# Optimization experiments

Hardware: AMD Instinct MI355X
Metric: run time of the kernel (lower is better)

## Reference

```python
import jax, jax.numpy as jnp
import numpy as np

B, T, H = 1, 2048, 2048
HEADS, DH = 16, 128  # head_dim = H // HEADS
K = 50               # block size
NEG = -1e9


def setup_inputs() -> dict:
    key = jax.random.key(0)
    ks = jax.random.split(key, 6)
    x = jax.random.normal(ks[0], (B, T, H), jnp.float32)
    mask = jnp.ones((B, T), jnp.float32)
    bias = jax.random.normal(ks[1], (B, HEADS, T, T), jnp.float32) * 0.02
    s = 1.0 / np.sqrt(H)
    Wq = jax.random.normal(ks[2], (H, HEADS, DH), jnp.float32) * s
    Wk = jax.random.normal(ks[3], (H, HEADS, DH), jnp.float32) * s
    Wv = jax.random.normal(ks[4], (H, HEADS, DH), jnp.float32) * s
    Wo = jax.random.normal(ks[5], (HEADS, DH, H), jnp.float32) * (1.0 / np.sqrt(H))
    return {"x_BxTxH": x, "mask_BxT": mask, "attention_bias_BxHxTxT": bias,
            "Wq": Wq, "Wk": Wk, "Wv": Wv, "Wo": Wo}


def _local_self_attention(x, mask, bias, Wq, Wk, Wv, Wo):
    b, t, h = x.shape
    extra = K - t % K          # module always pads (pads a full block if t % K == 0)
    p = t + extra
    n = p // K
    # pad + block the inputs: [b, n, K, h]
    xb = jnp.pad(x, ((0, 0), (0, extra), (0, 0))).reshape(b, n, K, h)
    # pad mask with -1e9 (as in the module), block, build pairwise mask via multiply
    mb = jnp.pad(mask, ((0, 0), (0, extra)), constant_values=NEG).reshape(b, n, K)
    pair = mb[..., :, None] * mb[..., None, :]              # [b, n, K, K]
    mask_bias = jnp.where(pair > 0, 0.0, NEG)[:, :, None]   # [b, n, 1, K, K] (broadcast heads)
    # pad attention bias and extract block-diagonal: [b, n, heads, K, K]
    bp = jnp.pad(bias, ((0, 0), (0, 0), (0, extra), (0, extra)))
    nb = bp.reshape(b, HEADS, n, K, n, K)
    idx = jnp.arange(n)
    blk_bias = nb[:, :, idx, :, idx, :]          # [n, b, heads, K, K]
    blk_bias = jnp.transpose(blk_bias, (1, 0, 2, 3, 4))  # [b, n, heads, K, K]
    # per-block multi-head attention (no qkv bias, query scaled by head_dim**-0.5)
    q = jnp.einsum('bnkh,hef->bnkef', xb, Wq) * (DH ** -0.5)
    k = jnp.einsum('bnkh,hef->bnkef', xb, Wk)
    v = jnp.einsum('bnkh,hef->bnkef', xb, Wv)
    logits = jnp.einsum('bnqef,bnkef->bneqk', q, k) + blk_bias + mask_bias
    attn = jax.nn.softmax(logits, axis=-1)
    out = jnp.einsum('bneqk,bnkef->bnqef', attn, v)
    out = jnp.einsum('bnqef,efh->bnqh', out, Wo).reshape(b, p, h)
    return out[:, :t, :]


def reference(x_BxTxH, mask_BxT, attention_bias_BxHxTxT, Wq, Wk, Wv, Wo):
    return _local_self_attention(x_BxTxH, mask_BxT, attention_bias_BxHxTxT, Wq, Wk, Wv, Wo)
```

## Files before the change

kernel.cpp:

```cpp
#include <hip/hip_runtime.h>
#include <hip/hip_bf16.h>

typedef _Float16 f16x8 __attribute__((ext_vector_type(8)));
typedef float f32x4 __attribute__((ext_vector_type(4)));

#define T_DIM 2048
#define H_DIM 2048
#define N_HEADS 16
#define DH 128
#define KBLK 50
#define NBLK 41
#define NEGV (-1.0e9f)
#define QSCALE 0.08838834764831845f

__device__ __forceinline__ void gl_lds16(const void* g, void* l) {
    __builtin_amdgcn_global_load_lds(
        (const __attribute__((address_space(1))) void*)g,
        (__attribute__((address_space(3))) void*)l, 16, 0, 0);
}

__global__ __launch_bounds__(256) void prep_kernel(const float* __restrict__ x,
                                                   const float* __restrict__ Wq,
                                                   const float* __restrict__ Wk,
                                                   const float* __restrict__ Wv,
                                                   const float* __restrict__ Wo,
                                                   _Float16* __restrict__ xb,
                                                   _Float16* __restrict__ WT,
                                                   _Float16* __restrict__ WoT) {
    __shared__ float tile[32][33];
    int z = blockIdx.z;
    int tx = threadIdx.x, ty = threadIdx.y;
    if (z == 4) {
        if (blockIdx.y >= 32) return;
        int flat = blockIdx.y * 64 + blockIdx.x;
        int i = (flat * 256 + ty * 32 + tx) * 8;
        float4 a = *(const float4*)&x[i];
        float4 b = *(const float4*)&x[i + 4];
        f16x8 o = {(_Float16)a.x, (_Float16)a.y, (_Float16)a.z, (_Float16)a.w,
                   (_Float16)b.x, (_Float16)b.y, (_Float16)b.z, (_Float16)b.w};
        *(f16x8*)&xb[i] = o;
        return;
    }
    const float* src = (z == 0) ? Wq : (z == 1) ? Wk : (z == 2) ? Wv : Wo;
    _Float16* dst = (z == 3) ? WoT : (WT + (size_t)z * T_DIM * H_DIM);
    int bx = blockIdx.x * 32, by = blockIdx.y * 32;
#pragma unroll
    for (int i = 0; i < 4; i++)
        tile[ty + i * 8][tx] = src[(size_t)(by + ty + i * 8) * H_DIM + bx + tx];
    __syncthreads();
#pragma unroll
    for (int i = 0; i < 4; i++)
        dst[(size_t)(bx + ty + i * 8) * H_DIM + by + tx] = (_Float16)tile[tx][ty + i * 8];
}

__global__ __launch_bounds__(512, 2) void qkv192_kernel(const _Float16* __restrict__ A,
                                                        const _Float16* __restrict__ BT,
                                                        _Float16* __restrict__ qkv) {
    const int K = 2048, NT = 32;
    __shared__ _Float16 smem[57344];
    _Float16* sA0 = smem;
    _Float16* sA1 = smem + 16384;
    _Float16* sB0 = smem + 32768;
    _Float16* sB1 = smem + 45056;

    int tid = threadIdx.x;
    int lane = tid & 63, wave = tid >> 6;
    int wm = wave >> 2, wn = wave & 3;
    int cb = lane & 15, hi = lane >> 4;

    int bid = blockIdx.x;
    int swz = (bid & 7) * 32 + (bid >> 3);
    int by = swz >> 5, bx = swz & 31;
    int bm = by * 256, bn = bx * 192;

    f32x4 acc[8][3];
#pragma unroll
    for (int m = 0; m < 8; m++)
#pragma unroll
        for (int n = 0; n < 3; n++) acc[m][n] = (f32x4){0.f, 0.f, 0.f, 0.f};

    int rp = tid >> 3, cc = tid & 7;
    int scol = ((cc ^ (rp & 7)) << 3);

    auto stageA = [&](int t, int u) {
        int buf = t & 1;
        gl_lds16(A + (size_t)(bm + u * 64 + rp) * K + (t << 6) + scol,
                 (buf ? sA1 : sA0) + u * 4096 + tid * 8);
    };
    auto stageB = [&](int t, int u) {
        int buf = t & 1;
        gl_lds16(BT + (size_t)(bn + u * 64 + rp) * K + (t << 6) + scol,
                 (buf ? sB1 : sB0) + u * 4096 + tid * 8);
    };

    f16x8 a_lo[4][2], a_hi[4][2], b01[2][2], b2[2];

    stageA(0, 0); stageA(0, 1); stageA(0, 2); stageA(0, 3);
    stageB(0, 0); stageB(0, 1); stageB(0, 2);
    stageA(1, 0); stageA(1, 1); stageA(1, 2); stageA(1, 3);
    asm volatile("s_waitcnt vmcnt(4)" ::: "memory");
    __builtin_amdgcn_s_barrier();

    for (int t = 0; t < NT; t++) {
        int buf = t & 1;
        const char* bA = (const char*)(buf ? sA1 : sA0);
        const char* bB = (const char*)(buf ? sB1 : sB0);
#pragma unroll
        for (int mf = 0; mf < 4; mf++) {
            int ra = wm * 128 + mf * 16 + cb;
#pragma unroll
            for (int ks = 0; ks < 2; ks++)
                a_lo[mf][ks] = *(const f16x8*)(bA + (ra << 7) +
                                               ((ks * 64 + hi * 16) ^ ((ra & 7) << 4)));
        }
#pragma unroll
        for (int nf = 0; nf < 2; nf++) {
            int rb = wn * 48 + nf * 16 + cb;
#pragma unroll
            for (int ks = 0; ks < 2; ks++)
                b01[nf][ks] = *(const f16x8*)(bB + (rb << 7) +
                                              ((ks * 64 + hi * 16) ^ ((rb & 7) << 4)));
        }
        if (t + 1 < NT) { stageB(t + 1, 0); stageB(t + 1, 1); }
        __builtin_amdgcn_s_barrier();
        asm volatile("s_waitcnt lgkmcnt(0)" ::: "memory");
        __builtin_amdgcn_s_setprio(1);
#pragma unroll
        for (int mf = 0; mf < 4; mf++)
#pragma unroll
            for (int nf = 0; nf < 2; nf++)
#pragma unroll
                for (int ks = 0; ks < 2; ks++)
                    acc[mf][nf] = __builtin_amdgcn_mfma_f32_16x16x32_f16(a_lo[mf][ks], b01[nf][ks], acc[mf][nf], 0, 0, 0);
        __builtin_amdgcn_s_setprio(0);
        __builtin_amdgcn_s_barrier();

#pragma unroll
        for (int mf = 0; mf < 4; mf++) {
            int ra = wm * 128 + 64 + mf * 16 + cb;
#pragma unroll
            for (int ks = 0; ks < 2; ks++)
                a_hi[mf][ks] = *(const f16x8*)(bA + (ra << 7) +
                                               ((ks * 64 + hi * 16) ^ ((ra & 7) << 4)));
        }
        {
            int rb = wn * 48 + 32 + cb;
#pragma unroll
            for (int ks = 0; ks < 2; ks++)
                b2[ks] = *(const f16x8*)(bB + (rb << 7) +
                                         ((ks * 64 + hi * 16) ^ ((rb & 7) << 4)));
        }
        if (t + 1 < NT) stageB(t + 1, 2);
        __builtin_amdgcn_s_barrier();
        asm volatile("s_waitcnt lgkmcnt(0)" ::: "memory");
        __builtin_amdgcn_s_setprio(1);
#pragma unroll
        for (int mf = 0; mf < 4; mf++)
#pragma unroll
            for (int ks = 0; ks < 2; ks++)
                acc[4 + mf][2] = __builtin_amdgcn_mfma_f32_16x16x32_f16(a_hi[mf][ks], b2[ks], acc[4 + mf][2], 0, 0, 0);
        __builtin_amdgcn_s_setprio(0);
        __builtin_amdgcn_s_barrier();

        if (t + 2 < NT) { stageA(t + 2, 0); stageA(t + 2, 1); }
        __builtin_amdgcn_s_barrier();
        __builtin_amdgcn_s_setprio(1);
#pragma unroll
        for (int mf = 0; mf < 4; mf++)
#pragma unroll
            for (int ks = 0; ks < 2; ks++)
                acc[mf][2] = __builtin_amdgcn_mfma_f32_16x16x32_f16(a_lo[mf][ks], b2[ks], acc[mf][2], 0, 0, 0);
        __builtin_amdgcn_s_setprio(0);
        __builtin_amdgcn_s_barrier();

        if (t + 2 < NT) { stageA(t + 2, 2); stageA(t + 2, 3); }
        if (t < NT - 2)
            asm volatile("s_waitcnt vmcnt(4)" ::: "memory");
        else if (t == NT - 2)
            asm volatile("s_waitcnt vmcnt(0)" ::: "memory");
        __builtin_amdgcn_s_barrier();
        __builtin_amdgcn_s_setprio(1);
#pragma unroll
        for (int mf = 0; mf < 4; mf++)
#pragma unroll
            for (int nf = 0; nf < 2; nf++)
#pragma unroll
                for (int ks = 0; ks < 2; ks++)
                    acc[4 + mf][nf] = __builtin_amdgcn_mfma_f32_16x16x32_f16(a_hi[mf][ks], b01[nf][ks], acc[4 + mf][nf], 0, 0, 0);
        __builtin_amdgcn_s_setprio(0);
        __builtin_amdgcn_s_barrier();
    }

#pragma unroll
    for (int p = 0; p < 2; p++) {
        if (p) __builtin_amdgcn_s_barrier();
        if (wm == p) {
#pragma unroll
            for (int mf = 0; mf < 8; mf++)
#pragma unroll
                for (int nf = 0; nf < 3; nf++) {
                    int col = wn * 48 + nf * 16 + cb;
                    float sc = ((bn + col) >> 11) == 0 ? QSCALE : 1.0f;
#pragma unroll
                    for (int r = 0; r < 4; r++) {
                        int row = mf * 16 + hi * 4 + r;
                        smem[row * 200 + col] = (_Float16)(acc[mf][nf][r] * sc);
                    }
                }
        }
        __builtin_amdgcn_s_barrier();
#pragma unroll
        for (int it = 0; it < 6; it++) {
            int c = it * 512 + tid;
            int row = c / 24, col8 = c - row * 24;
            int gm = bm + p * 128 + row;
            int gn = bn + col8 * 8;
            int tensor = gn >> 11;
            int ef = gn & 2047;
            int e = ef >> 7, f0 = ef & 127;
            uint4 v = *(const uint4*)&smem[row * 200 + col8 * 8];
            *(uint4*)(qkv + (size_t)tensor * (T_DIM * H_DIM) + (size_t)e * (T_DIM * DH) +
                      (size_t)gm * DH + f0) = v;
        }
    }
}

__global__ __launch_bounds__(512, 1) void oproj_kernel(const _Float16* __restrict__ A,
                                                       const _Float16* __restrict__ BT,
                                                       float* __restrict__ out) {
    const int K = 2048, NT = 32;
    __shared__ _Float16 smem[49152];

    int tid = threadIdx.x;
    int lane = tid & 63, wave = tid >> 6;
    int wm = wave >> 2, wn = wave & 3;
    int cb = lane & 15, hi = lane >> 4;

    int bid = blockIdx.x;
    int by = bid >> 4, bx = bid & 15;
    int bm = by * 128, bn = bx * 128;

    f32x4 acc[4][2];
#pragma unroll
    for (int m = 0; m < 4; m++)
#pragma unroll
        for (int n = 0; n < 2; n++) acc[m][n] = (f32x4){0.f, 0.f, 0.f, 0.f};

    int rp = tid >> 3, cc = tid & 7;
    int scol = ((cc ^ (rp & 7)) << 3);

    auto bufp = [&](int t) { return smem + (t % 3) * 16384; };
    auto stageA = [&](int t, int u) {
        gl_lds16(A + (size_t)(bm + u * 64 + rp) * K + (t << 6) + scol,
                 bufp(t) + u * 4096 + tid * 8);
    };
    auto stageB = [&](int t, int u) {
        gl_lds16(BT + (size_t)(bn + u * 64 + rp) * K + (t << 6) + scol,
                 bufp(t) + 8192 + u * 4096 + tid * 8);
    };

    f16x8 a[4][2], b0[2], b1[2];

    stageA(0, 0); stageA(0, 1); stageB(0, 0); stageB(0, 1);
    stageA(1, 0); stageA(1, 1); stageB(1, 0); stageB(1, 1);
    asm volatile("s_waitcnt vmcnt(4)" ::: "memory");
    __builtin_amdgcn_s_barrier();

    for (int t = 0; t < NT; t++) {
        const char* bA = (const char*)bufp(t);
        const char* bB = bA + 16384;
#pragma unroll
        for (int mf = 0; mf < 4; mf++) {
            int ra = wm * 64 + mf * 16 + cb;
#pragma unroll
            for (int ks = 0; ks < 2; ks++)
                a[mf][ks] = *(const f16x8*)(bA + (ra << 7) +
                                            ((ks * 64 + hi * 16) ^ ((ra & 7) << 4)));
        }
        {
            int rb = wn * 32 + cb;
#pragma unroll
            for (int ks = 0; ks < 2; ks++)
                b0[ks] = *(const f16x8*)(bB + (rb << 7) +
                                         ((ks * 64 + hi * 16) ^ ((rb & 7) << 4)));
        }
        if (t + 2 < NT) { stageA(t + 2, 0); stageA(t + 2, 1); }
        __builtin_amdgcn_s_barrier();
        asm volatile("s_waitcnt lgkmcnt(0)" ::: "memory");
        __builtin_amdgcn_s_setprio(1);
#pragma unroll
        for (int mf = 0; mf < 4; mf++)
#pragma unroll
            for (int ks = 0; ks < 2; ks++)
                acc[mf][0] = __builtin_amdgcn_mfma_f32_16x16x32_f16(a[mf][ks], b0[ks], acc[mf][0], 0, 0, 0);
        __builtin_amdgcn_s_setprio(0);
        __builtin_amdgcn_s_barrier();

        {
            int rb = wn * 32 + 16 + cb;
#pragma unroll
            for (int ks = 0; ks < 2; ks++)
                b1[ks] = *(const f16x8*)(bB + (rb << 7) +
                                         ((ks * 64 + hi * 16) ^ ((rb & 7) << 4)));
        }
        if (t + 2 < NT) { stageB(t + 2, 0); stageB(t + 2, 1); }
        if (t < NT - 2)
            asm volatile("s_waitcnt vmcnt(4)" ::: "memory");
        else if (t == NT - 2)
            asm volatile("s_waitcnt vmcnt(0)" ::: "memory");
        __builtin_amdgcn_s_barrier();
        asm volatile("s_waitcnt lgkmcnt(0)" ::: "memory");
        __builtin_amdgcn_s_setprio(1);
#pragma unroll
        for (int mf = 0; mf < 4; mf++)
#pragma unroll
            for (int ks = 0; ks < 2; ks++)
                acc[mf][1] = __builtin_amdgcn_mfma_f32_16x16x32_f16(a[mf][ks], b1[ks], acc[mf][1], 0, 0, 0);
        __builtin_amdgcn_s_setprio(0);
        __builtin_amdgcn_s_barrier();
    }

#pragma unroll
    for (int mf = 0; mf < 4; mf++)
#pragma unroll
        for (int nf = 0; nf < 2; nf++) {
            int gn = bn + wn * 32 + nf * 16 + cb;
#pragma unroll
            for (int r = 0; r < 4; r++) {
                int gm = bm + wm * 64 + mf * 16 + hi * 4 + r;
                out[(size_t)gm * H_DIM + gn] = acc[mf][nf][r];
            }
        }
}

__global__ __launch_bounds__(256) void attn_kernel(const _Float16* __restrict__ qkvb,
                                                   const float* __restrict__ bias,
                                                   const float* __restrict__ mask,
                                                   _Float16* __restrict__ aout) {
    int bid = blockIdx.x;
    int n = bid >> 4, e = bid & 15;
    int t0 = n * KBLK;
    int valid = (T_DIM - t0 < KBLK) ? (T_DIM - t0) : KBLK;

    __shared__ _Float16 Qs[64 * 136];
    __shared__ _Float16 Ks[64 * 136];
    __shared__ _Float16 VTs[128 * 72];
    __shared__ _Float16 Ps[64 * 72];
    __shared__ float maskv[64];

    int tid = threadIdx.x;
    int lane = tid & 63, wave = tid >> 6;
    const _Float16* qp = qkvb + (size_t)e * (T_DIM * DH);
    const _Float16* kp = qkvb + (size_t)(T_DIM * H_DIM) + (size_t)e * (T_DIM * DH);
    const _Float16* vp = qkvb + (size_t)2 * (T_DIM * H_DIM) + (size_t)e * (T_DIM * DH);

#pragma unroll
    for (int i = 0; i < 4; i++) {
        int c = tid + i * 256;
        int r = c >> 4, c8 = c & 15;
        uint4 z = {0u, 0u, 0u, 0u};
        uint4 vq = z, vk = z;
        if (r < valid) {
            vq = *(const uint4*)&qp[(size_t)(t0 + r) * DH + c8 * 8];
            vk = *(const uint4*)&kp[(size_t)(t0 + r) * DH + c8 * 8];
        }
        *(uint4*)&Qs[r * 136 + c8 * 8] = vq;
        *(uint4*)&Ks[r * 136 + c8 * 8] = vk;
    }
#pragma unroll
    for (int i = 0; i < 4; i++) {
        int c = tid + i * 256;
        int r = c & 63;
        int f0 = (c >> 6) * 8;
        uint4 v = {0u, 0u, 0u, 0u};
        if (r < valid) v = *(const uint4*)&vp[(size_t)(t0 + r) * DH + f0];
        _Float16 tmp[8];
        *(uint4*)tmp = v;
#pragma unroll
        for (int j = 0; j < 8; j++) VTs[(f0 + j) * 72 + r] = tmp[j];
    }
    if (tid < 64) maskv[tid] = (tid < valid) ? mask[t0 + tid] : NEGV;
    __syncthreads();

    int qr0 = wave * 16;
    int cb = lane & 15, hi = lane >> 4;

    f16x8 aq[4];
#pragma unroll
    for (int ks = 0; ks < 4; ks++)
        aq[ks] = *(const f16x8*)&Qs[(qr0 + cb) * 136 + ks * 32 + hi * 8];
    f32x4 s[4];
#pragma unroll
    for (int kt = 0; kt < 4; kt++) s[kt] = (f32x4){0.f, 0.f, 0.f, 0.f};
#pragma unroll
    for (int kt = 0; kt < 4; kt++)
#pragma unroll
        for (int ks = 0; ks < 4; ks++) {
            f16x8 bk = *(const f16x8*)&Ks[(kt * 16 + cb) * 136 + ks * 32 + hi * 8];
            s[kt] = __builtin_amdgcn_mfma_f32_16x16x32_f16(aq[ks], bk, s[kt], 0, 0, 0);
        }

#pragma unroll
    for (int r = 0; r < 4; r++) {
        int rl = qr0 + hi * 4 + r;
        int qi = t0 + rl;
        float mq = maskv[rl];
        float lg[4];
        float mx = -3.4e38f;
#pragma unroll
        for (int kt = 0; kt < 4; kt++) {
            int cl = kt * 16 + cb, ki = t0 + cl;
            float bg = (qi < T_DIM && ki < T_DIM)
                           ? bias[((size_t)e * T_DIM + qi) * T_DIM + ki] : 0.f;
            float pr = mq * maskv[cl];
            float v = s[kt][r] + bg + (pr > 0.f ? 0.f : NEGV);
            lg[kt] = v;
            mx = fmaxf(mx, v);
        }
#pragma unroll
        for (int off = 8; off; off >>= 1) mx = fmaxf(mx, __shfl_xor(mx, off));
        float sum = 0.f;
#pragma unroll
        for (int kt = 0; kt < 4; kt++) {
            float pe = __expf(lg[kt] - mx);
            lg[kt] = pe;
            sum += pe;
        }
#pragma unroll
        for (int off = 8; off; off >>= 1) sum += __shfl_xor(sum, off);
        float inv = 1.f / sum;
#pragma unroll
        for (int kt = 0; kt < 4; kt++)
            Ps[rl * 72 + kt * 16 + cb] = (_Float16)(lg[kt] * inv);
    }
    __syncthreads();

    f16x8 pa[2];
#pragma unroll
    for (int ks = 0; ks < 2; ks++)
        pa[ks] = *(const f16x8*)&Ps[(qr0 + cb) * 72 + ks * 32 + hi * 8];
#pragma unroll
    for (int ft = 0; ft < 8; ft++) {
        f32x4 o = (f32x4){0.f, 0.f, 0.f, 0.f};
#pragma unroll
        for (int ks = 0; ks < 2; ks++) {
            f16x8 bv = *(const f16x8*)&VTs[(ft * 16 + cb) * 72 + ks * 32 + hi * 8];
            o = __builtin_amdgcn_mfma_f32_16x16x32_f16(pa[ks], bv, o, 0, 0, 0);
        }
#pragma unroll
        for (int r = 0; r < 4; r++) {
            int rl = qr0 + hi * 4 + r;
            if (rl < valid)
                aout[(size_t)(t0 + rl) * H_DIM + e * DH + ft * 16 + cb] = (_Float16)o[r];
        }
    }
}

extern "C" void kernel_launch(void* const* d_in, const int* in_sizes, int n_in,
                              void* d_out, int out_size, void* d_ws, size_t ws_size,
                              hipStream_t stream) {
    const float* x    = (const float*)d_in[0];
    const float* mask = (const float*)d_in[1];
    const float* bias = (const float*)d_in[2];
    const float* Wq   = (const float*)d_in[3];
    const float* Wk   = (const float*)d_in[4];
    const float* Wv   = (const float*)d_in[5];
    const float* Wo   = (const float*)d_in[6];
    float* out = (float*)d_out;

    _Float16* xb   = (_Float16*)d_ws;
    _Float16* WT   = xb + (size_t)T_DIM * H_DIM;
    _Float16* WoT  = WT + (size_t)3 * T_DIM * H_DIM;
    _Float16* qkvb = WoT + (size_t)T_DIM * H_DIM;
    _Float16* aout = qkvb + (size_t)3 * T_DIM * H_DIM;

    prep_kernel<<<dim3(64, 64, 5), dim3(32, 8), 0, stream>>>(x, Wq, Wk, Wv, Wo, xb, WT, WoT);

    qkv192_kernel<<<256, 512, 0, stream>>>(xb, WT, qkvb);

    attn_kernel<<<NBLK * N_HEADS, 256, 0, stream>>>(qkvb, bias, mask, aout);

    oproj_kernel<<<256, 512, 0, stream>>>(aout, WoT, out);
}
```

Baseline: 119.4 us.

## Shrink QKV and output-projection GEMM tiles to 256-thread blocks with more CTAs

The QKV GEMM moves from 256x192 tiles with 512 threads to 128x192 tiles with 256 threads (2x2 waves, each 64x96). The output projection moves from 128x128 tiles to 128x64 tiles. Both now launch 512 blocks and are tuned for two blocks per CU. The goal is more CTAs, better spread across the GPU's CUs, and less LDS per block, at the cost of lower arithmetic intensity per tile and more global traffic. The QKV block-index swizzle is dropped, and the epilogue is simplified to a single pass through shared memory.

```diff
diff --git a/kernel.cpp b/kernel.cpp
--- a/kernel.cpp
+++ b/kernel.cpp
@@ -53,50 +53,47 @@
         dst[(size_t)(bx + ty + i * 8) * H_DIM + by + tx] = (_Float16)tile[tx][ty + i * 8];
 }
 
-__global__ __launch_bounds__(512, 2) void qkv192_kernel(const _Float16* __restrict__ A,
-                                                        const _Float16* __restrict__ BT,
-                                                        _Float16* __restrict__ qkv) {
+__global__ __launch_bounds__(256, 2) void qkv_kernel(const _Float16* __restrict__ A,
+                                                     const _Float16* __restrict__ BT,
+                                                     _Float16* __restrict__ qkv) {
     const int K = 2048, NT = 32;
-    __shared__ _Float16 smem[57344];
+    __shared__ _Float16 smem[40960];
     _Float16* sA0 = smem;
-    _Float16* sA1 = smem + 16384;
-    _Float16* sB0 = smem + 32768;
-    _Float16* sB1 = smem + 45056;
+    _Float16* sA1 = smem + 8192;
+    _Float16* sB0 = smem + 16384;
+    _Float16* sB1 = smem + 28672;
 
     int tid = threadIdx.x;
     int lane = tid & 63, wave = tid >> 6;
-    int wm = wave >> 2, wn = wave & 3;
+    int wm = wave >> 1, wn = wave & 1;
     int cb = lane & 15, hi = lane >> 4;
 
     int bid = blockIdx.x;
-    int swz = (bid & 7) * 32 + (bid >> 3);
-    int by = swz >> 5, bx = swz & 31;
-    int bm = by * 256, bn = bx * 192;
-
-    f32x4 acc[8][3];
-#pragma unroll
-    for (int m = 0; m < 8; m++)
-#pragma unroll
-        for (int n = 0; n < 3; n++) acc[m][n] = (f32x4){0.f, 0.f, 0.f, 0.f};
+    int by = bid >> 5, bx = bid & 31;
+    int bm = by * 128, bn = bx * 192;
+
+    f32x4 acc[4][6];
+#pragma unroll
+    for (int m = 0; m < 4; m++)
+#pragma unroll
+        for (int n = 0; n < 6; n++) acc[m][n] = (f32x4){0.f, 0.f, 0.f, 0.f};
 
     int rp = tid >> 3, cc = tid & 7;
     int scol = ((cc ^ (rp & 7)) << 3);
 
     auto stageA = [&](int t, int u) {
-        int buf = t & 1;
-        gl_lds16(A + (size_t)(bm + u * 64 + rp) * K + (t << 6) + scol,
-                 (buf ? sA1 : sA0) + u * 4096 + tid * 8);
+        gl_lds16(A + (size_t)(bm + u * 32 + rp) * K + (t << 6) + scol,
+                 ((t & 1) ? sA1 : sA0) + u * 2048 + tid * 8);
     };
     auto stageB = [&](int t, int u) {
-        int buf = t & 1;
-        gl_lds16(BT + (size_t)(bn + u * 64 + rp) * K + (t << 6) + scol,
-                 (buf ? sB1 : sB0) + u * 4096 + tid * 8);
+        gl_lds16(BT + (size_t)(bn + u * 32 + rp) * K + (t << 6) + scol,
+                 ((t & 1) ? sB1 : sB0) + u * 2048 + tid * 8);
     };
 
-    f16x8 a_lo[4][2], a_hi[4][2], b01[2][2], b2[2];
+    f16x8 a[4][2], b[6][2];
 
     stageA(0, 0); stageA(0, 1); stageA(0, 2); stageA(0, 3);
-    stageB(0, 0); stageB(0, 1); stageB(0, 2);
+    stageB(0, 0); stageB(0, 1); stageB(0, 2); stageB(0, 3); stageB(0, 4); stageB(0, 5);
     stageA(1, 0); stageA(1, 1); stageA(1, 2); stageA(1, 3);
     asm volatile("s_waitcnt vmcnt(4)" ::: "memory");
     __builtin_amdgcn_s_barrier();
@@ -107,58 +104,53 @@
         const char* bB = (const char*)(buf ? sB1 : sB0);
 #pragma unroll
         for (int mf = 0; mf < 4; mf++) {
-            int ra = wm * 128 + mf * 16 + cb;
-#pragma unroll
-            for (int ks = 0; ks < 2; ks++)
-                a_lo[mf][ks] = *(const f16x8*)(bA + (ra << 7) +
-                                               ((ks * 64 + hi * 16) ^ ((ra & 7) << 4)));
-        }
-#pragma unroll
-        for (int nf = 0; nf < 2; nf++) {
-            int rb = wn * 48 + nf * 16 + cb;
-#pragma unroll
-            for (int ks = 0; ks < 2; ks++)
-                b01[nf][ks] = *(const f16x8*)(bB + (rb << 7) +
-                                              ((ks * 64 + hi * 16) ^ ((rb & 7) << 4)));
-        }
-        if (t + 1 < NT) { stageB(t + 1, 0); stageB(t + 1, 1); }
+            int ra = wm * 64 + mf * 16 + cb;
+#pragma unroll
+            for (int ks = 0; ks < 2; ks++)
+                a[mf][ks] = *(const f16x8*)(bA + (ra << 7) +
+                                            ((ks * 64 + hi * 16) ^ ((ra & 7) << 4)));
+        }
+#pragma unroll
+        for (int nf = 0; nf < 3; nf++) {
+            int rb = wn * 96 + nf * 16 + cb;
+#pragma unroll
+            for (int ks = 0; ks < 2; ks++)
+                b[nf][ks] = *(const f16x8*)(bB + (rb << 7) +
+                                            ((ks * 64 + hi * 16) ^ ((rb & 7) << 4)));
+        }
+        if (t + 1 < NT) { stageB(t + 1, 0); stageB(t + 1, 1); stageB(t + 1, 2); }
         __builtin_amdgcn_s_barrier();
         asm volatile("s_waitcnt lgkmcnt(0)" ::: "memory");
         __builtin_amdgcn_s_setprio(1);
 #pragma unroll
-        for (int mf = 0; mf < 4; mf++)
-#pragma unroll
-            for (int nf = 0; nf < 2; nf++)
+        for (int mf = 0; mf < 2; mf++)
+#pragma unroll
+            for (int nf = 0; nf < 3; nf++)
 #pragma unroll
                 for (int ks = 0; ks < 2; ks++)
-                    acc[mf][nf] = __builtin_amdgcn_mfma_f32_16x16x32_f16(a_lo[mf][ks], b01[nf][ks], acc[mf][nf], 0, 0, 0);
-        __builtin_amdgcn_s_setprio(0);
-        __builtin_amdgcn_s_barrier();
-
-#pragma unroll
-        for (int mf = 0; mf < 4; mf++) {
-            int ra = wm * 128 + 64 + mf * 16 + cb;
-#pragma unroll
-            for (int ks = 0; ks < 2; ks++)
-                a_hi[mf][ks] = *(const f16x8*)(bA + (ra << 7) +
-                                               ((ks * 64 + hi * 16) ^ ((ra & 7) << 4)));
-        }
-        {
-            int rb = wn * 48 + 32 + cb;
-#pragma unroll
-            for (int ks = 0; ks < 2; ks++)
-                b2[ks] = *(const f16x8*)(bB + (rb << 7) +
-                                         ((ks * 64 + hi * 16) ^ ((rb & 7) << 4)));
-        }
-        if (t + 1 < NT) stageB(t + 1, 2);
+                    acc[mf][nf] = __builtin_amdgcn_mfma_f32_16x16x32_f16(a[mf][ks], b[nf][ks], acc[mf][nf], 0, 0, 0);
+        __builtin_amdgcn_s_setprio(0);
+        __builtin_amdgcn_s_barrier();
+
+#pragma unroll
+        for (int nf = 3; nf < 6; nf++) {
+            int rb = wn * 96 + nf * 16 + cb;
+#pragma unroll
+            for (int ks = 0; ks < 2; ks++)
+                b[nf][ks] = *(const f16x8*)(bB + (rb << 7) +
+                                            ((ks * 64 + hi * 16) ^ ((rb & 7) << 4)));
+        }
+        if (t + 1 < NT) { stageB(t + 1, 3); stageB(t + 1, 4); stageB(t + 1, 5); }
         __builtin_amdgcn_s_barrier();
         asm volatile("s_waitcnt lgkmcnt(0)" ::: "memory");
         __builtin_amdgcn_s_setprio(1);
 #pragma unroll
-        for (int mf = 0; mf < 4; mf++)
-#pragma unroll
-            for (int ks = 0; ks < 2; ks++)
-                acc[4 + mf][2] = __builtin_amdgcn_mfma_f32_16x16x32_f16(a_hi[mf][ks], b2[ks], acc[4 + mf][2], 0, 0, 0);
+        for (int mf = 0; mf < 2; mf++)
+#pragma unroll
+            for (int nf = 3; nf < 6; nf++)
+#pragma unroll
+                for (int ks = 0; ks < 2; ks++)
+                    acc[mf][nf] = __builtin_amdgcn_mfma_f32_16x16x32_f16(a[mf][ks], b[nf][ks], acc[mf][nf], 0, 0, 0);
         __builtin_amdgcn_s_setprio(0);
         __builtin_amdgcn_s_barrier();
 
@@ -166,10 +158,12 @@
         __builtin_amdgcn_s_barrier();
         __builtin_amdgcn_s_setprio(1);
 #pragma unroll
-        for (int mf = 0; mf < 4; mf++)
-#pragma unroll
-            for (int ks = 0; ks < 2; ks++)
-                acc[mf][2] = __builtin_amdgcn_mfma_f32_16x16x32_f16(a_lo[mf][ks], b2[ks], acc[mf][2], 0, 0, 0);
+        for (int mf = 2; mf < 4; mf++)
+#pragma unroll
+            for (int nf = 0; nf < 3; nf++)
+#pragma unroll
+                for (int ks = 0; ks < 2; ks++)
+                    acc[mf][nf] = __builtin_amdgcn_mfma_f32_16x16x32_f16(a[mf][ks], b[nf][ks], acc[mf][nf], 0, 0, 0);
         __builtin_amdgcn_s_setprio(0);
         __builtin_amdgcn_s_barrier();
 
@@ -181,64 +175,58 @@
         __builtin_amdgcn_s_barrier();
         __builtin_amdgcn_s_setprio(1);
 #pragma unroll
-        for (int mf = 0; mf < 4; mf++)
-#pragma unroll
-            for (int nf = 0; nf < 2; nf++)
+        for (int mf = 2; mf < 4; mf++)
+#pragma unroll
+            for (int nf = 3; nf < 6; nf++)
 #pragma unroll
                 for (int ks = 0; ks < 2; ks++)
-                    acc[4 + mf][nf] = __builtin_amdgcn_mfma_f32_16x16x32_f16(a_hi[mf][ks], b01[nf][ks], acc[4 + mf][nf], 0, 0, 0);
-        __builtin_amdgcn_s_setprio(0);
-        __builtin_amdgcn_s_barrier();
-    }
-
-#pragma unroll
-    for (int p = 0; p < 2; p++) {
-        if (p) __builtin_amdgcn_s_barrier();
-        if (wm == p) {
-#pragma unroll
-            for (int mf = 0; mf < 8; mf++)
-#pragma unroll
-                for (int nf = 0; nf < 3; nf++) {
-                    int col = wn * 48 + nf * 16 + cb;
-                    float sc = ((bn + col) >> 11) == 0 ? QSCALE : 1.0f;
-#pragma unroll
-                    for (int r = 0; r < 4; r++) {
-                        int row = mf * 16 + hi * 4 + r;
-                        smem[row * 200 + col] = (_Float16)(acc[mf][nf][r] * sc);
-                    }
-                }
-        }
-        __builtin_amdgcn_s_barrier();
-#pragma unroll
-        for (int it = 0; it < 6; it++) {
-            int c = it * 512 + tid;
-            int row = c / 24, col8 = c - row * 24;
-            int gm = bm + p * 128 + row;
-            int gn = bn + col8 * 8;
-            int tensor = gn >> 11;
-            int ef = gn & 2047;
-            int e = ef >> 7, f0 = ef & 127;
-            uint4 v = *(const uint4*)&smem[row * 200 + col8 * 8];
-            *(uint4*)(qkv + (size_t)tensor * (T_DIM * H_DIM) + (size_t)e * (T_DIM * DH) +
-                      (size_t)gm * DH + f0) = v;
-        }
-    }
-}
-
-__global__ __launch_bounds__(512, 1) void oproj_kernel(const _Float16* __restrict__ A,
+                    acc[mf][nf] = __builtin_amdgcn_mfma_f32_16x16x32_f16(a[mf][ks], b[nf][ks], acc[mf][nf], 0, 0, 0);
+        __builtin_amdgcn_s_setprio(0);
+        __builtin_amdgcn_s_barrier();
+    }
+
+#pragma unroll
+    for (int mf = 0; mf < 4; mf++)
+#pragma unroll
+        for (int nf = 0; nf < 6; nf++) {
+            int col = wn * 96 + nf * 16 + cb;
+            float sc = ((bn + col) >> 11) == 0 ? QSCALE : 1.0f;
+#pragma unroll
+            for (int r = 0; r < 4; r++) {
+                int row = wm * 64 + mf * 16 + hi * 4 + r;
+                smem[row * 200 + col] = (_Float16)(acc[mf][nf][r] * sc);
+            }
+        }
+    __builtin_amdgcn_s_barrier();
+#pragma unroll
+    for (int it = 0; it < 12; it++) {
+        int c = it * 256 + tid;
+        int row = c / 24, col8 = c - row * 24;
+        int gm = bm + row;
+        int gn = bn + col8 * 8;
+        int tensor = gn >> 11;
+        int ef = gn & 2047;
+        int e = ef >> 7, f0 = ef & 127;
+        uint4 v = *(const uint4*)&smem[row * 200 + col8 * 8];
+        *(uint4*)(qkv + (size_t)tensor * (T_DIM * H_DIM) + (size_t)e * (T_DIM * DH) +
+                  (size_t)gm * DH + f0) = v;
+    }
+}
+
+__global__ __launch_bounds__(256, 2) void oproj_kernel(const _Float16* __restrict__ A,
                                                        const _Float16* __restrict__ BT,
                                                        float* __restrict__ out) {
     const int K = 2048, NT = 32;
-    __shared__ _Float16 smem[49152];
+    __shared__ _Float16 smem[36864];
 
     int tid = threadIdx.x;
     int lane = tid & 63, wave = tid >> 6;
-    int wm = wave >> 2, wn = wave & 3;
+    int wm = wave >> 1, wn = wave & 1;
     int cb = lane & 15, hi = lane >> 4;
 
     int bid = blockIdx.x;
-    int by = bid >> 4, bx = bid & 15;
-    int bm = by * 128, bn = bx * 128;
+    int by = bid >> 5, bx = bid & 31;
+    int bm = by * 128, bn = bx * 64;
 
     f32x4 acc[4][2];
 #pragma unroll
@@ -249,21 +237,21 @@
     int rp = tid >> 3, cc = tid & 7;
     int scol = ((cc ^ (rp & 7)) << 3);
 
-    auto bufp = [&](int t) { return smem + (t % 3) * 16384; };
+    auto bufp = [&](int t) { return smem + (t % 3) * 12288; };
     auto stageA = [&](int t, int u) {
-        gl_lds16(A + (size_t)(bm + u * 64 + rp) * K + (t << 6) + scol,
-                 bufp(t) + u * 4096 + tid * 8);
+        gl_lds16(A + (size_t)(bm + u * 32 + rp) * K + (t << 6) + scol,
+                 bufp(t) + u * 2048 + tid * 8);
     };
     auto stageB = [&](int t, int u) {
-        gl_lds16(BT + (size_t)(bn + u * 64 + rp) * K + (t << 6) + scol,
-                 bufp(t) + 8192 + u * 4096 + tid * 8);
+        gl_lds16(BT + (size_t)(bn + u * 32 + rp) * K + (t << 6) + scol,
+                 bufp(t) + 8192 + u * 2048 + tid * 8);
     };
 
     f16x8 a[4][2], b0[2], b1[2];
 
-    stageA(0, 0); stageA(0, 1); stageB(0, 0); stageB(0, 1);
-    stageA(1, 0); stageA(1, 1); stageB(1, 0); stageB(1, 1);
-    asm volatile("s_waitcnt vmcnt(4)" ::: "memory");
+    stageA(0, 0); stageA(0, 1); stageA(0, 2); stageA(0, 3); stageB(0, 0); stageB(0, 1);
+    stageA(1, 0); stageA(1, 1); stageA(1, 2); stageA(1, 3); stageB(1, 0); stageB(1, 1);
+    asm volatile("s_waitcnt vmcnt(6)" ::: "memory");
     __builtin_amdgcn_s_barrier();
 
     for (int t = 0; t < NT; t++) {
@@ -284,7 +272,7 @@
                 b0[ks] = *(const f16x8*)(bB + (rb << 7) +
                                          ((ks * 64 + hi * 16) ^ ((rb & 7) << 4)));
         }
-        if (t + 2 < NT) { stageA(t + 2, 0); stageA(t + 2, 1); }
+        if (t + 2 < NT) { stageA(t + 2, 0); stageA(t + 2, 1); stageA(t + 2, 2); stageA(t + 2, 3); }
         __builtin_amdgcn_s_barrier();
         asm volatile("s_waitcnt lgkmcnt(0)" ::: "memory");
         __builtin_amdgcn_s_setprio(1);
@@ -305,7 +293,7 @@
         }
         if (t + 2 < NT) { stageB(t + 2, 0); stageB(t + 2, 1); }
         if (t < NT - 2)
-            asm volatile("s_waitcnt vmcnt(4)" ::: "memory");
+            asm volatile("s_waitcnt vmcnt(6)" ::: "memory");
         else if (t == NT - 2)
             asm volatile("s_waitcnt vmcnt(0)" ::: "memory");
         __builtin_amdgcn_s_barrier();
@@ -476,9 +464,9 @@
 
     prep_kernel<<<dim3(64, 64, 5), dim3(32, 8), 0, stream>>>(x, Wq, Wk, Wv, Wo, xb, WT, WoT);
 
-    qkv192_kernel<<<256, 512, 0, stream>>>(xb, WT, qkvb);
+    qkv_kernel<<<512, 256, 0, stream>>>(xb, WT, qkvb);
 
     attn_kernel<<<NBLK * N_HEADS, 256, 0, stream>>>(qkvb, bias, mask, aout);
 
-    oproj_kernel<<<256, 512, 0, stream>>>(aout, WoT, out);
-}
+    oproj_kernel<<<512, 256, 0, stream>>>(aout, WoT, out);
+}
```

Result: faster. 116.3 us (-2.6%).
